# Performance work log

Measured on AMD Instinct MI355X. Metric: run time of the kernel, lower is better.

The kernel has to match this reference:

```python
import jax, jax.numpy as jnp
import numpy as np

B, C, H, W = 8, 512, 64, 64


def _conv1x1(x, w, b):
    # x: (B,C,H,W), w: (O,C,1,1) torch layout, b: (O,)
    y = jnp.einsum('bchw,oc->bohw', x, w[:, :, 0, 0])
    return y + b[None, :, None, None]


def setup_inputs() -> dict:
    key = jax.random.key(0)
    ks = jax.random.split(key, 9)
    s = 1.0 / np.sqrt(C)
    inp = {
        'x': jax.random.normal(ks[0], (B, C, H, W), dtype=jnp.float32),
        'w1': jax.random.uniform(ks[1], (C, C, 1, 1), jnp.float32, -s, s),
        'b1': jax.random.uniform(ks[2], (C,), jnp.float32, -s, s),
        'w2': jax.random.uniform(ks[3], (C, C, 1, 1), jnp.float32, -s, s),
        'b2': jax.random.uniform(ks[4], (C,), jnp.float32, -s, s),
        'w3': jax.random.uniform(ks[5], (C, C, 1, 1), jnp.float32, -s, s),
        'b3': jax.random.uniform(ks[6], (C,), jnp.float32, -s, s),
        'wg': jax.random.uniform(ks[7], (C, 1, 3, 3), jnp.float32, -1.0 / 3.0, 1.0 / 3.0),
        'bg': jax.random.uniform(ks[8], (C,), jnp.float32, -1.0 / 3.0, 1.0 / 3.0),
    }
    return inp


def reference(x, w1, b1, w2, b2, w3, b3, wg, bg):
    q = _conv1x1(x, w1, b1)  # (B,C,H,W)
    k = _conv1x1(x, w2, b2)
    v = _conv1x1(x, w3, b3)
    qf = q.reshape(B, C, H * W)
    kf = k.reshape(B, C, H * W)
    vf = v.reshape(B, C, H * W)
    # channel-wise attention: (B,C,C)
    scores = jnp.einsum('bcn,bdn->bcd', qf, kf)
    attn = jax.nn.softmax(scores, axis=-1)
    denoised = jnp.einsum('bcd,bdn->bcn', attn, vf).reshape(B, C, H, W)
    # depthwise 3x3 conv, padding=1
    local = jax.lax.conv_general_dilated(
        x, wg, window_strides=(1, 1), padding=((1, 1), (1, 1)),
        feature_group_count=C,
        dimension_numbers=('NCHW', 'OIHW', 'NCHW'))
    local = local + bg[None, :, None, None]
    return x + 0.1 * denoised + 0.1 * local
```

## Files before the change

kernel.cpp:

```cpp
#include <hip/hip_runtime.h>

typedef _Float16 f16;
typedef _Float16 half8 __attribute__((ext_vector_type(8)));
typedef _Float16 half4 __attribute__((ext_vector_type(4)));
typedef float    f32x4 __attribute__((ext_vector_type(4)));

#define DEV static __device__ __forceinline__

constexpr int NB = 8, CH = 512, HW = 4096, IH = 64, IW = 64;

typedef const __attribute__((address_space(1))) void gas_void;
typedef __attribute__((address_space(3))) void       las_void;

template <int ROWS>
DEV void stage_gll(f16* lds, const f16* src, long ld) {
  const int lane = threadIdx.x & 63, w = threadIdx.x >> 6;
  const int r8 = lane >> 3, c16 = lane & 7;
#pragma unroll
  for (int i = w; i < (ROWS / 8); i += 4) {
    const f16* g = src + (long)(i * 8 + r8) * ld + c16 * 8;
    __builtin_amdgcn_global_load_lds((gas_void*)g, (las_void*)(lds + i * 512 + lane * 8), 16, 0, 0);
  }
}

template <int BM, int BN, bool SPLIT, int KS, int EPI, bool TRI>
__global__ __launch_bounds__(256, 2) void gemm2(
    const f16* __restrict__ Ah, const f16* __restrict__ Al, long sAb, int lda,
    const f16* __restrict__ Bh, const f16* __restrict__ Bl, long sBb, int ldb,
    void* __restrict__ O1, void* __restrict__ O2, long sOb, int ldo, int K,
    const float* __restrict__ e0, const float* __restrict__ e1,
    const float* __restrict__ e2, const float* __restrict__ e3) {
  constexpr int FM = BM / 32, FN = BN / 32;
  __shared__ f16 sAh[BM * 64], sBh[BN * 64];
  __shared__ f16 sAl[SPLIT ? BM * 64 : 1], sBl[SPLIT ? BN * 64 : 1];

  int bx = blockIdx.x, by = blockIdx.y;
  if constexpr (TRI) {
    int t = blockIdx.x, mi = 0;
    while (t >= 4 - mi) { t -= 4 - mi; ++mi; }
    bx = mi; by = mi + t;
  }
  const int bz = blockIdx.z, b = bz / KS, ks = bz % KS;
  const int m0 = bx * BM, n0 = by * BN;
  const int lane = threadIdx.x & 63, wave = threadIdx.x >> 6;
  const int wr = (wave >> 1) * (BM / 2), wc = (wave & 1) * (BN / 2);
  const int fr = lane & 15, fq = lane >> 4;

  const f16* Ab  = Ah + b * sAb + (long)m0 * lda;
  const f16* Bb  = Bh + b * sBb + (long)n0 * ldb;
  const f16* Ab2 = SPLIT ? Al + b * sAb + (long)m0 * lda : nullptr;
  const f16* Bb2 = SPLIT ? Bl + b * sBb + (long)n0 * ldb : nullptr;

  f32x4 acc[FM][FN] = {};
  const int kbeg = ks * K, kend = kbeg + K;
  for (int k0 = kbeg; k0 < kend; k0 += 64) {
    stage_gll<BM>(sAh, Ab + k0, lda);
    stage_gll<BN>(sBh, Bb + k0, ldb);
    if constexpr (SPLIT) {
      stage_gll<BM>(sAl, Ab2 + k0, lda);
      stage_gll<BN>(sBl, Bb2 + k0, ldb);
    }
    __syncthreads();
#pragma unroll
    for (int kk = 0; kk < 2; ++kk) {
      half8 ah[FM], bh[FN];
#pragma unroll
      for (int mi = 0; mi < FM; ++mi)
        ah[mi] = *(const half8*)&sAh[(wr + mi * 16 + fr) * 64 + kk * 32 + fq * 8];
#pragma unroll
      for (int ni = 0; ni < FN; ++ni)
        bh[ni] = *(const half8*)&sBh[(wc + ni * 16 + fr) * 64 + kk * 32 + fq * 8];
      if constexpr (SPLIT) {
        half8 al[FM], bl[FN];
#pragma unroll
        for (int mi = 0; mi < FM; ++mi)
          al[mi] = *(const half8*)&sAl[(wr + mi * 16 + fr) * 64 + kk * 32 + fq * 8];
#pragma unroll
        for (int ni = 0; ni < FN; ++ni)
          bl[ni] = *(const half8*)&sBl[(wc + ni * 16 + fr) * 64 + kk * 32 + fq * 8];
#pragma unroll
        for (int mi = 0; mi < FM; ++mi)
#pragma unroll
          for (int ni = 0; ni < FN; ++ni) {
            acc[mi][ni] = __builtin_amdgcn_mfma_f32_16x16x32_f16(ah[mi], bh[ni], acc[mi][ni], 0, 0, 0);
            acc[mi][ni] = __builtin_amdgcn_mfma_f32_16x16x32_f16(ah[mi], bl[ni], acc[mi][ni], 0, 0, 0);
            acc[mi][ni] = __builtin_amdgcn_mfma_f32_16x16x32_f16(al[mi], bh[ni], acc[mi][ni], 0, 0, 0);
          }
      } else {
#pragma unroll
        for (int mi = 0; mi < FM; ++mi)
#pragma unroll
          for (int ni = 0; ni < FN; ++ni)
            acc[mi][ni] = __builtin_amdgcn_mfma_f32_16x16x32_f16(ah[mi], bh[ni], acc[mi][ni], 0, 0, 0);
      }
    }
    __syncthreads();
  }

#pragma unroll
  for (int mi = 0; mi < FM; ++mi)
#pragma unroll
    for (int ni = 0; ni < FN; ++ni)
#pragma unroll
      for (int j = 0; j < 4; ++j) {
        const int row = m0 + wr + mi * 16 + fq * 4 + j;
        const int col = n0 + wc + ni * 16 + fr;
        float g = acc[mi][ni][j];
        const long oi = b * sOb + (long)row * ldo + col;
        if constexpr (EPI == 0) {
          f16 h = (f16)g;
          ((f16*)O1)[oi] = h;
          ((f16*)O2)[oi] = (f16)(g - (float)h);
        } else if constexpr (EPI == 1) {
          g += e0[row] * e1[b * CH + col] + e2[b * CH + row] * e3[col];
          ((float*)O1)[oi] = g;
        } else if constexpr (EPI == 2) {
          ((f16*)O1)[oi] = (f16)g;
        } else if constexpr (EPI == 3) {
          ((float*)O1)[oi] += 0.1f * (g + e1[b * CH + row]);
        } else {
          unsafeAtomicAdd(&((float*)O1)[oi], g);
        }
      }
}

template <int OP>
DEV float blockReduce(float v) {
#pragma unroll
  for (int o = 32; o; o >>= 1) {
    float w = __shfl_xor(v, o);
    v = OP ? fmaxf(v, w) : v + w;
  }
  __shared__ float t[4];
  __shared__ float res;
  __syncthreads();
  if ((threadIdx.x & 63) == 0) t[threadIdx.x >> 6] = v;
  __syncthreads();
  if (threadIdx.x == 0)
    res = OP ? fmaxf(fmaxf(t[0], t[1]), fmaxf(t[2], t[3])) : t[0] + t[1] + t[2] + t[3];
  __syncthreads();
  return res;
}

__global__ __launch_bounds__(256) void convert_x(const float* __restrict__ x, f16* __restrict__ xh,
                                                 f16* __restrict__ xl, f16* __restrict__ xT) {
  const int p0 = blockIdx.x * 64, c0 = blockIdx.y * 64, b = blockIdx.z;
  __shared__ f16 tl[64][72];
  const int t = threadIdx.x;
  const int rr0 = t >> 4, c4 = (t & 15) * 4;
  const float* xb = x + (long)b * CH * HW;
#pragma unroll
  for (int i = 0; i < 4; ++i) {
    const int r = rr0 + i * 16;
    f32x4 v = *(const f32x4*)(xb + (long)(c0 + r) * HW + p0 + c4);
    half4 h, l;
#pragma unroll
    for (int j = 0; j < 4; ++j) {
      f16 hi = (f16)v[j];
      h[j] = hi;
      l[j] = (f16)(v[j] - (float)hi);
      tl[c4 + j][r] = hi;
    }
    *(half4*)(xh + ((long)b * CH + c0 + r) * HW + p0 + c4) = h;
    *(half4*)(xl + ((long)b * CH + c0 + r) * HW + p0 + c4) = l;
  }
  __syncthreads();
  const int pr = t >> 2, cc = (t & 3) * 16;
  f16* dst = xT + ((long)b * HW + p0 + pr) * CH + c0 + cc;
  *(half8*)dst       = *(half8*)&tl[pr][cc];
  *(half8*)(dst + 8) = *(half8*)&tl[pr][cc + 8];
}

__global__ __launch_bounds__(256) void cvt_g(const float* __restrict__ G32, f16* __restrict__ Gh,
                                             f16* __restrict__ Gl) {
  const int c0 = blockIdx.x * 64, r0 = blockIdx.y * 64, b = blockIdx.z;
  const bool lower = (r0 >> 7) > (c0 >> 7);
  __shared__ float tl[64][65];
  const int t = threadIdx.x;
  const int rr0 = t >> 4, c4 = (t & 15) * 4;
  const float* Gb = G32 + (long)b * CH * CH;
  if (lower) {
#pragma unroll
    for (int i = 0; i < 4; ++i) {
      const int r = rr0 + i * 16;
      f32x4 v = *(const f32x4*)(Gb + (long)(c0 + r) * CH + r0 + c4);
#pragma unroll
      for (int j = 0; j < 4; ++j) tl[c4 + j][r] = v[j];
    }
    __syncthreads();
  }
#pragma unroll
  for (int i = 0; i < 4; ++i) {
    const int r = rr0 + i * 16;
    f32x4 v;
    if (lower)
      v = *(const f32x4*)&tl[r][c4];
    else
      v = *(const f32x4*)(Gb + (long)(r0 + r) * CH + c0 + c4);
    half4 h, l;
#pragma unroll
    for (int j = 0; j < 4; ++j) {
      f16 hi = (f16)v[j];
      h[j] = hi;
      l[j] = (f16)(v[j] - (float)hi);
    }
    *(half4*)(Gh + ((long)b * CH + r0 + r) * CH + c0 + c4) = h;
    *(half4*)(Gl + ((long)b * CH + r0 + r) * CH + c0 + c4) = l;
  }
}

__global__ __launch_bounds__(256) void prep_w(const float* __restrict__ w1, const float* __restrict__ w2,
                                              const float* __restrict__ w3, f16* w1h, f16* w1l, f16* w2h,
                                              f16* w2l, f16* w3t) {
  const int i = blockIdx.x * 256 + threadIdx.x;
  if (i >= CH * CH) return;
  float a = w1[i];
  f16 h = (f16)a;
  w1h[i] = h;
  w1l[i] = (f16)(a - (float)h);
  float bv = w2[i];
  h = (f16)bv;
  w2h[i] = h;
  w2l[i] = (f16)(bv - (float)h);
  const int r = i >> 9, c = i & 511;
  w3t[c * CH + r] = (f16)w3[i];
}

__global__ __launch_bounds__(256) void rowsum_k(const float* __restrict__ x, float* __restrict__ s) {
  const int b = blockIdx.y, c = blockIdx.x;
  const float* p = x + ((long)(b * CH + c)) * HW;
  float a = 0.f;
  for (int i = threadIdx.x; i < HW; i += 256) a += p[i];
  a = blockReduce<0>(a);
  if (threadIdx.x == 0) s[b * CH + c] = a;
}

__global__ __launch_bounds__(256) void prep_tu(const float* __restrict__ w1, const float* __restrict__ w2,
                                               const float* __restrict__ b2, const float* __restrict__ s,
                                               float* __restrict__ t, float* __restrict__ u) {
  const int b = blockIdx.y, c = blockIdx.x;
  float a1 = 0.f, a2 = 0.f;
  for (int i = threadIdx.x; i < CH; i += 256) {
    float sv = s[b * CH + i];
    a1 += w1[(long)c * CH + i] * sv;
    a2 += w2[(long)c * CH + i] * sv;
  }
  a1 = blockReduce<0>(a1);
  a2 = blockReduce<0>(a2);
  if (threadIdx.x == 0) {
    t[b * CH + c] = a1;
    u[b * CH + c] = a2 + (float)HW * b2[c];
  }
}

__global__ __launch_bounds__(256) void softmax_k(const float* __restrict__ sc, const float* __restrict__ b3,
                                                 f16* __restrict__ attn, float* __restrict__ ab3) {
  const int b = blockIdx.y, c = blockIdx.x;
  const float* row = sc + ((long)(b * CH + c)) * CH;
  const float v0 = row[threadIdx.x], v1 = row[threadIdx.x + 256];
  const float m = blockReduce<1>(fmaxf(v0, v1));
  const float q0 = __expf(v0 - m), q1 = __expf(v1 - m);
  const float sum = blockReduce<0>(q0 + q1);
  const float sb = blockReduce<0>(q0 * b3[threadIdx.x] + q1 * b3[threadIdx.x + 256]);
  const float inv = 1.f / sum;
  attn[((long)(b * CH + c)) * CH + threadIdx.x] = (f16)(q0 * inv);
  attn[((long)(b * CH + c)) * CH + threadIdx.x + 256] = (f16)(q1 * inv);
  if (threadIdx.x == 0) ab3[b * CH + c] = sb * inv;
}

__global__ __launch_bounds__(256) void dwconv_k(const float* __restrict__ x, const float* __restrict__ wg,
                                                const float* __restrict__ bg, float* __restrict__ out) {
  const int b = blockIdx.y, c = blockIdx.x;
  __shared__ float img[IH][IW + 1];
  const float* p = x + ((long)(b * CH + c)) * HW;
  for (int i = threadIdx.x; i < HW; i += 256) img[i >> 6][i & 63] = p[i];
  __syncthreads();
  float w[3][3];
#pragma unroll
  for (int k = 0; k < 9; ++k) w[k / 3][k % 3] = wg[c * 9 + k];
  const float bias = bg[c];
  float* op = out + ((long)(b * CH + c)) * HW;
  for (int i = threadIdx.x; i < HW; i += 256) {
    const int h = i >> 6, ww = i & 63;
    float acc = bias;
#pragma unroll
    for (int dy = -1; dy <= 1; ++dy) {
      const int hh = h + dy;
      if (hh < 0 || hh >= IH) continue;
#pragma unroll
      for (int dx = -1; dx <= 1; ++dx) {
        const int cc2 = ww + dx;
        if (cc2 < 0 || cc2 >= IW) continue;
        acc += w[dy + 1][dx + 1] * img[hh][cc2];
      }
    }
    op[i] = img[h][ww] + 0.1f * acc;
  }
}

extern "C" void kernel_launch(void* const* d_in, const int* in_sizes, int n_in, void* d_out, int out_size,
                              void* d_ws, size_t ws_size, hipStream_t stream) {
  const float* x  = (const float*)d_in[0];
  const float* w1 = (const float*)d_in[1];
  const float* b1 = (const float*)d_in[2];
  const float* w2 = (const float*)d_in[3];
  const float* b2 = (const float*)d_in[4];
  const float* w3 = (const float*)d_in[5];
  const float* b3 = (const float*)d_in[6];
  const float* wg = (const float*)d_in[7];
  const float* bg = (const float*)d_in[8];
  float* out = (float*)d_out;

  char* ws = (char*)d_ws;
  size_t off = 0;
  auto alloc = [&](size_t bytes) -> void* {
    void* p = ws + off;
    off += (bytes + 255) & ~(size_t)255;
    return p;
  };
  const long CC = (long)CH * CH;
  const long CHW = (long)CH * HW;
  f16* xh  = (f16*)alloc(NB * CHW * 2);
  f16* xl  = (f16*)alloc(NB * CHW * 2);
  f16* xT  = (f16*)alloc(NB * CHW * 2);
  float* G32 = (float*)alloc(NB * CC * 4);
  f16* G16h = (f16*)alloc(NB * CC * 2);
  f16* G16l = (f16*)alloc(NB * CC * 2);
  f16* P16h = (f16*)alloc(NB * CC * 2);
  f16* P16l = (f16*)alloc(NB * CC * 2);
  f16* w1h = (f16*)alloc(CC * 2);
  f16* w1l = (f16*)alloc(CC * 2);
  f16* w2h = (f16*)alloc(CC * 2);
  f16* w2l = (f16*)alloc(CC * 2);
  f16* w3t = (f16*)alloc(CC * 2);
  float* sv = (float*)alloc(NB * CH * 4);
  float* tv = (float*)alloc(NB * CH * 4);
  float* uv = (float*)alloc(NB * CH * 4);
  float* ab3 = (float*)alloc(NB * CH * 4);
  float* scores = G32;
  f16* attn16 = G16h;
  f16* M16    = G16l;

  const dim3 blk(256);

  prep_w<<<dim3((CH * CH + 255) / 256), blk, 0, stream>>>(w1, w2, w3, w1h, w1l, w2h, w2l, w3t);
  convert_x<<<dim3(HW / 64, CH / 64, NB), blk, 0, stream>>>(x, xh, xl, xT);
  rowsum_k<<<dim3(CH, NB), blk, 0, stream>>>(x, sv);
  prep_tu<<<dim3(CH, NB), blk, 0, stream>>>(w1, w2, b2, sv, tv, uv);
  hipMemsetAsync(G32, 0, NB * CC * 4, stream);

  gemm2<128, 128, true, 8, 5, true><<<dim3(10, 1, NB * 8), blk, 0, stream>>>(
      xh, xl, CHW, HW, xh, xl, CHW, HW, G32, nullptr, CC, CH, HW / 8,
      nullptr, nullptr, nullptr, nullptr);
  cvt_g<<<dim3(8, 8, NB), blk, 0, stream>>>(G32, G16h, G16l);
  gemm2<128, 64, true, 1, 0, false><<<dim3(4, 8, NB), blk, 0, stream>>>(
      w1h, w1l, 0, CH, G16h, G16l, CC, CH, P16h, P16l, CC, CH, CH,
      nullptr, nullptr, nullptr, nullptr);
  gemm2<128, 64, true, 1, 1, false><<<dim3(4, 8, NB), blk, 0, stream>>>(
      P16h, P16l, CC, CH, w2h, w2l, 0, CH, scores, nullptr, CC, CH, CH, b1, uv, tv, b2);
  softmax_k<<<dim3(CH, NB), blk, 0, stream>>>(scores, b3, attn16, ab3);
  gemm2<128, 64, false, 1, 2, false><<<dim3(4, 8, NB), blk, 0, stream>>>(
      attn16, nullptr, CC, CH, w3t, nullptr, 0, CH, M16, nullptr, CC, CH, CH,
      nullptr, nullptr, nullptr, nullptr);
  dwconv_k<<<dim3(CH, NB), blk, 0, stream>>>(x, wg, bg, out);
  gemm2<128, 128, false, 1, 3, false><<<dim3(4, HW / 128, NB), blk, 0, stream>>>(
      M16, nullptr, CC, CH, xT, nullptr, CHW, CH, out, nullptr, CHW, HW, CH,
      nullptr, ab3, nullptr, nullptr);
}
```

Before: 381.7 us.

## Fuse rowsum into convert_x, reuse A tile on diagonal, fold dwconv into combine

The per-channel row sums move into convert_x as shuffle reductions plus atomics, which removes a separate full pass over x. Diagonal blocks of the symmetric Gram GEMM reuse the A tile in LDS for B instead of loading the same data twice. The final GEMM now writes the denoised result to an fp16 buffer (reusing xl), and a new combine kernel adds it to the depthwise conv, bias and residual. This drops the read-modify-write of out inside the GEMM epilogue, at the cost of an extra fp16 intermediate round trip and some precision loss from rounding the denoised term to fp16.

```diff
diff --git a/kernel.cpp b/kernel.cpp
--- a/kernel.cpp
+++ b/kernel.cpp
@@ -40,6 +40,7 @@
     while (t >= 4 - mi) { t -= 4 - mi; ++mi; }
     bx = mi; by = mi + t;
   }
+  const bool diag = TRI && (bx == by);
   const int bz = blockIdx.z, b = bz / KS, ks = bz % KS;
   const int m0 = bx * BM, n0 = by * BN;
   const int lane = threadIdx.x & 63, wave = threadIdx.x >> 6;
@@ -51,14 +52,17 @@
   const f16* Ab2 = SPLIT ? Al + b * sAb + (long)m0 * lda : nullptr;
   const f16* Bb2 = SPLIT ? Bl + b * sBb + (long)n0 * ldb : nullptr;
 
+  const f16* pBh = diag ? sAh : sBh;
+  const f16* pBl = diag ? sAl : sBl;
+
   f32x4 acc[FM][FN] = {};
   const int kbeg = ks * K, kend = kbeg + K;
   for (int k0 = kbeg; k0 < kend; k0 += 64) {
     stage_gll<BM>(sAh, Ab + k0, lda);
-    stage_gll<BN>(sBh, Bb + k0, ldb);
+    if (!diag) stage_gll<BN>(sBh, Bb + k0, ldb);
     if constexpr (SPLIT) {
       stage_gll<BM>(sAl, Ab2 + k0, lda);
-      stage_gll<BN>(sBl, Bb2 + k0, ldb);
+      if (!diag) stage_gll<BN>(sBl, Bb2 + k0, ldb);
     }
     __syncthreads();
 #pragma unroll
@@ -69,7 +73,7 @@
         ah[mi] = *(const half8*)&sAh[(wr + mi * 16 + fr) * 64 + kk * 32 + fq * 8];
 #pragma unroll
       for (int ni = 0; ni < FN; ++ni)
-        bh[ni] = *(const half8*)&sBh[(wc + ni * 16 + fr) * 64 + kk * 32 + fq * 8];
+        bh[ni] = *(const half8*)&pBh[(wc + ni * 16 + fr) * 64 + kk * 32 + fq * 8];
       if constexpr (SPLIT) {
         half8 al[FM], bl[FN];
 #pragma unroll
@@ -77,7 +81,7 @@
           al[mi] = *(const half8*)&sAl[(wr + mi * 16 + fr) * 64 + kk * 32 + fq * 8];
 #pragma unroll
         for (int ni = 0; ni < FN; ++ni)
-          bl[ni] = *(const half8*)&sBl[(wc + ni * 16 + fr) * 64 + kk * 32 + fq * 8];
+          bl[ni] = *(const half8*)&pBl[(wc + ni * 16 + fr) * 64 + kk * 32 + fq * 8];
 #pragma unroll
         for (int mi = 0; mi < FM; ++mi)
 #pragma unroll
@@ -116,8 +120,6 @@
           ((float*)O1)[oi] = g;
         } else if constexpr (EPI == 2) {
           ((f16*)O1)[oi] = (f16)g;
-        } else if constexpr (EPI == 3) {
-          ((float*)O1)[oi] += 0.1f * (g + e1[b * CH + row]);
         } else {
           unsafeAtomicAdd(&((float*)O1)[oi], g);
         }
@@ -143,7 +145,8 @@
 }
 
 __global__ __launch_bounds__(256) void convert_x(const float* __restrict__ x, f16* __restrict__ xh,
-                                                 f16* __restrict__ xl, f16* __restrict__ xT) {
+                                                 f16* __restrict__ xl, f16* __restrict__ xT,
+                                                 float* __restrict__ sv) {
   const int p0 = blockIdx.x * 64, c0 = blockIdx.y * 64, b = blockIdx.z;
   __shared__ f16 tl[64][72];
   const int t = threadIdx.x;
@@ -163,6 +166,12 @@
     }
     *(half4*)(xh + ((long)b * CH + c0 + r) * HW + p0 + c4) = h;
     *(half4*)(xl + ((long)b * CH + c0 + r) * HW + p0 + c4) = l;
+    float s4 = v[0] + v[1] + v[2] + v[3];
+    s4 += __shfl_xor(s4, 1);
+    s4 += __shfl_xor(s4, 2);
+    s4 += __shfl_xor(s4, 4);
+    s4 += __shfl_xor(s4, 8);
+    if ((t & 15) == 0) unsafeAtomicAdd(&sv[(long)b * CH + c0 + r], s4);
   }
   __syncthreads();
   const int pr = t >> 2, cc = (t & 3) * 16;
@@ -226,15 +235,6 @@
   w3t[c * CH + r] = (f16)w3[i];
 }
 
-__global__ __launch_bounds__(256) void rowsum_k(const float* __restrict__ x, float* __restrict__ s) {
-  const int b = blockIdx.y, c = blockIdx.x;
-  const float* p = x + ((long)(b * CH + c)) * HW;
-  float a = 0.f;
-  for (int i = threadIdx.x; i < HW; i += 256) a += p[i];
-  a = blockReduce<0>(a);
-  if (threadIdx.x == 0) s[b * CH + c] = a;
-}
-
 __global__ __launch_bounds__(256) void prep_tu(const float* __restrict__ w1, const float* __restrict__ w2,
                                                const float* __restrict__ b2, const float* __restrict__ s,
                                                float* __restrict__ t, float* __restrict__ u) {
@@ -268,8 +268,9 @@
   if (threadIdx.x == 0) ab3[b * CH + c] = sb * inv;
 }
 
-__global__ __launch_bounds__(256) void dwconv_k(const float* __restrict__ x, const float* __restrict__ wg,
-                                                const float* __restrict__ bg, float* __restrict__ out) {
+__global__ __launch_bounds__(256) void combine_k(const float* __restrict__ x, const f16* __restrict__ den,
+                                                 const float* __restrict__ wg, const float* __restrict__ bg,
+                                                 const float* __restrict__ ab3, float* __restrict__ out) {
   const int b = blockIdx.y, c = blockIdx.x;
   __shared__ float img[IH][IW + 1];
   const float* p = x + ((long)(b * CH + c)) * HW;
@@ -278,11 +279,12 @@
   float w[3][3];
 #pragma unroll
   for (int k = 0; k < 9; ++k) w[k / 3][k % 3] = wg[c * 9 + k];
-  const float bias = bg[c];
+  const float base = bg[c] + ab3[b * CH + c];
+  const f16* dp = den + ((long)(b * CH + c)) * HW;
   float* op = out + ((long)(b * CH + c)) * HW;
   for (int i = threadIdx.x; i < HW; i += 256) {
     const int h = i >> 6, ww = i & 63;
-    float acc = bias;
+    float acc = base + (float)dp[i];
 #pragma unroll
     for (int dy = -1; dy <= 1; ++dy) {
       const int hh = h + dy;
@@ -340,12 +342,13 @@
   float* scores = G32;
   f16* attn16 = G16h;
   f16* M16    = G16l;
+  f16* den16  = xl;
 
   const dim3 blk(256);
 
   prep_w<<<dim3((CH * CH + 255) / 256), blk, 0, stream>>>(w1, w2, w3, w1h, w1l, w2h, w2l, w3t);
-  convert_x<<<dim3(HW / 64, CH / 64, NB), blk, 0, stream>>>(x, xh, xl, xT);
-  rowsum_k<<<dim3(CH, NB), blk, 0, stream>>>(x, sv);
+  hipMemsetAsync(sv, 0, NB * CH * 4, stream);
+  convert_x<<<dim3(HW / 64, CH / 64, NB), blk, 0, stream>>>(x, xh, xl, xT, sv);
   prep_tu<<<dim3(CH, NB), blk, 0, stream>>>(w1, w2, b2, sv, tv, uv);
   hipMemsetAsync(G32, 0, NB * CC * 4, stream);
 
@@ -362,8 +365,8 @@
   gemm2<128, 64, false, 1, 2, false><<<dim3(4, 8, NB), blk, 0, stream>>>(
       attn16, nullptr, CC, CH, w3t, nullptr, 0, CH, M16, nullptr, CC, CH, CH,
       nullptr, nullptr, nullptr, nullptr);
-  dwconv_k<<<dim3(CH, NB), blk, 0, stream>>>(x, wg, bg, out);
-  gemm2<128, 128, false, 1, 3, false><<<dim3(4, HW / 128, NB), blk, 0, stream>>>(
-      M16, nullptr, CC, CH, xT, nullptr, CHW, CH, out, nullptr, CHW, HW, CH,
-      nullptr, ab3, nullptr, nullptr);
-}
+  gemm2<128, 128, false, 1, 2, false><<<dim3(4, HW / 128, NB), blk, 0, stream>>>(
+      M16, nullptr, CC, CH, xT, nullptr, CHW, CH, den16, nullptr, CHW, HW, CH,
+      nullptr, nullptr, nullptr, nullptr);
+  combine_k<<<dim3(CH, NB), blk, 0, stream>>>(x, den16, wg, bg, ab3, out);
+}
```

Result: faster. 344.5 us (-9.8%).

## Compute Gram matrix with single fp16 GEMM using hi/mid split and partial buffers

Applied to the files above, without the earlier changes.

Replaces the split-precision triangular Gram GEMM (hi/lo for both operands, atomics into a zeroed buffer) with one non-split GEMM of xh against xm, where xm = 2x - xh. This makes xh·xm + xm·xh ≈ 2·x·x^T once symmetrised. Split-K partials go to separate buffers and cvt_g sums them with their transposes. The row-sum is fused into the conversion kernel, and the final GEMM writes denoised fp16 into a combine kernel that also applies the depthwise conv and bias. The aim is to cut GEMM work, the memset and the atomics. The trade-offs are a full (non-triangular) grid, extra partial-buffer traffic and fp16 rounding of xm and of the denoised output.

```diff
diff --git a/kernel.cpp b/kernel.cpp
--- a/kernel.cpp
+++ b/kernel.cpp
@@ -23,7 +23,7 @@
   }
 }
 
-template <int BM, int BN, bool SPLIT, int KS, int EPI, bool TRI>
+template <int BM, int BN, bool SPLIT, int KS, int EPI>
 __global__ __launch_bounds__(256, 2) void gemm2(
     const f16* __restrict__ Ah, const f16* __restrict__ Al, long sAb, int lda,
     const f16* __restrict__ Bh, const f16* __restrict__ Bl, long sBb, int ldb,
@@ -34,12 +34,7 @@
   __shared__ f16 sAh[BM * 64], sBh[BN * 64];
   __shared__ f16 sAl[SPLIT ? BM * 64 : 1], sBl[SPLIT ? BN * 64 : 1];
 
-  int bx = blockIdx.x, by = blockIdx.y;
-  if constexpr (TRI) {
-    int t = blockIdx.x, mi = 0;
-    while (t >= 4 - mi) { t -= 4 - mi; ++mi; }
-    bx = mi; by = mi + t;
-  }
+  const int bx = blockIdx.x, by = blockIdx.y;
   const int bz = blockIdx.z, b = bz / KS, ks = bz % KS;
   const int m0 = bx * BM, n0 = by * BN;
   const int lane = threadIdx.x & 63, wave = threadIdx.x >> 6;
@@ -116,10 +111,8 @@
           ((float*)O1)[oi] = g;
         } else if constexpr (EPI == 2) {
           ((f16*)O1)[oi] = (f16)g;
-        } else if constexpr (EPI == 3) {
-          ((float*)O1)[oi] += 0.1f * (g + e1[b * CH + row]);
         } else {
-          unsafeAtomicAdd(&((float*)O1)[oi], g);
+          ((float*)O1)[(((long)ks * NB + b) * CH + row) * CH + col] = g;
         }
       }
 }
@@ -142,70 +135,90 @@
   return res;
 }
 
-__global__ __launch_bounds__(256) void convert_x(const float* __restrict__ x, f16* __restrict__ xh,
-                                                 f16* __restrict__ xl, f16* __restrict__ xT) {
+__global__ __launch_bounds__(256) void convert1(const float* __restrict__ x, f16* __restrict__ xh,
+                                                f16* __restrict__ xm, float* __restrict__ sv) {
+  const int c = blockIdx.x, b = blockIdx.y;
+  const long base = ((long)(b * CH + c)) * HW;
+  const float* p = x + base;
+  f16* ph = xh + base;
+  f16* pm = xm + base;
+  float s = 0.f;
+#pragma unroll
+  for (int i0 = 0; i0 < 4; ++i0) {
+    const int i = (threadIdx.x + i0 * 256) * 4;
+    f32x4 v = *(const f32x4*)(p + i);
+    half4 h, m;
+#pragma unroll
+    for (int j = 0; j < 4; ++j) {
+      f16 hi = (f16)v[j];
+      h[j] = hi;
+      m[j] = (f16)(2.f * v[j] - (float)hi);
+      s += v[j];
+    }
+    *(half4*)(ph + i) = h;
+    *(half4*)(pm + i) = m;
+  }
+  s = blockReduce<0>(s);
+  if (threadIdx.x == 0) sv[b * CH + c] = s;
+}
+
+__global__ __launch_bounds__(256) void convert2(const f16* __restrict__ xh, f16* __restrict__ xT) {
   const int p0 = blockIdx.x * 64, c0 = blockIdx.y * 64, b = blockIdx.z;
   __shared__ f16 tl[64][72];
   const int t = threadIdx.x;
-  const int rr0 = t >> 4, c4 = (t & 15) * 4;
-  const float* xb = x + (long)b * CH * HW;
-#pragma unroll
-  for (int i = 0; i < 4; ++i) {
-    const int r = rr0 + i * 16;
-    f32x4 v = *(const f32x4*)(xb + (long)(c0 + r) * HW + p0 + c4);
-    half4 h, l;
-#pragma unroll
-    for (int j = 0; j < 4; ++j) {
-      f16 hi = (f16)v[j];
-      h[j] = hi;
-      l[j] = (f16)(v[j] - (float)hi);
-      tl[c4 + j][r] = hi;
-    }
-    *(half4*)(xh + ((long)b * CH + c0 + r) * HW + p0 + c4) = h;
-    *(half4*)(xl + ((long)b * CH + c0 + r) * HW + p0 + c4) = l;
-  }
-  __syncthreads();
-  const int pr = t >> 2, cc = (t & 3) * 16;
-  f16* dst = xT + ((long)b * HW + p0 + pr) * CH + c0 + cc;
-  *(half8*)dst       = *(half8*)&tl[pr][cc];
-  *(half8*)(dst + 8) = *(half8*)&tl[pr][cc + 8];
-}
-
-__global__ __launch_bounds__(256) void cvt_g(const float* __restrict__ G32, f16* __restrict__ Gh,
+  const int cr = t >> 2, pc = (t & 3) * 16;
+  const f16* src = xh + ((long)(b * CH) + c0 + cr) * HW + p0 + pc;
+  half8 a0 = *(const half8*)src, a1 = *(const half8*)(src + 8);
+#pragma unroll
+  for (int j = 0; j < 8; ++j) {
+    tl[pc + j][cr] = a0[j];
+    tl[pc + 8 + j][cr] = a1[j];
+  }
+  __syncthreads();
+  f16* dst = xT + ((long)b * HW + p0 + cr) * CH + c0 + pc;
+  *(half8*)dst       = *(half8*)&tl[cr][pc];
+  *(half8*)(dst + 8) = *(half8*)&tl[cr][pc + 8];
+}
+
+template <int KS>
+__global__ __launch_bounds__(256) void cvt_g(const float* __restrict__ E, f16* __restrict__ Gh,
                                              f16* __restrict__ Gl) {
   const int c0 = blockIdx.x * 64, r0 = blockIdx.y * 64, b = blockIdx.z;
-  const bool lower = (r0 >> 7) > (c0 >> 7);
   __shared__ float tl[64][65];
   const int t = threadIdx.x;
   const int rr0 = t >> 4, c4 = (t & 15) * 4;
-  const float* Gb = G32 + (long)b * CH * CH;
-  if (lower) {
+  f32x4 acc[4] = {};
+  for (int ks = 0; ks < KS; ++ks) {
+    const float* Eb = E + ((long)ks * NB + b) * (long)CH * CH;
+#pragma unroll
+    for (int i = 0; i < 4; ++i)
+      acc[i] += *(const f32x4*)(Eb + (long)(r0 + rr0 + i * 16) * CH + c0 + c4);
+    __syncthreads();
 #pragma unroll
     for (int i = 0; i < 4; ++i) {
-      const int r = rr0 + i * 16;
-      f32x4 v = *(const f32x4*)(Gb + (long)(c0 + r) * CH + r0 + c4);
-#pragma unroll
-      for (int j = 0; j < 4; ++j) tl[c4 + j][r] = v[j];
+      f32x4 w = *(const f32x4*)(Eb + (long)(c0 + rr0 + i * 16) * CH + r0 + c4);
+#pragma unroll
+      for (int j = 0; j < 4; ++j) tl[rr0 + i * 16][c4 + j] = w[j];
     }
     __syncthreads();
+#pragma unroll
+    for (int i = 0; i < 4; ++i)
+#pragma unroll
+      for (int j = 0; j < 4; ++j) acc[i][j] += tl[c4 + j][rr0 + i * 16];
   }
 #pragma unroll
   for (int i = 0; i < 4; ++i) {
-    const int r = rr0 + i * 16;
-    f32x4 v;
-    if (lower)
-      v = *(const f32x4*)&tl[r][c4];
-    else
-      v = *(const f32x4*)(Gb + (long)(r0 + r) * CH + c0 + c4);
     half4 h, l;
 #pragma unroll
     for (int j = 0; j < 4; ++j) {
-      f16 hi = (f16)v[j];
+      const float g = 0.5f * acc[i][j];
+      f16 hi = (f16)g;
       h[j] = hi;
-      l[j] = (f16)(v[j] - (float)hi);
-    }
-    *(half4*)(Gh + ((long)b * CH + r0 + r) * CH + c0 + c4) = h;
-    *(half4*)(Gl + ((long)b * CH + r0 + r) * CH + c0 + c4) = l;
+      l[j] = (f16)(g - (float)hi);
+    }
+    const long oi = ((long)b * CH + r0 + rr0 + i * 16) * CH + c0 + c4;
+    *(half4*)(Gh + oi) = h;
+    *(half4*)(Gl + oi) = l;
   }
 }
 
@@ -226,15 +239,6 @@
   w3t[c * CH + r] = (f16)w3[i];
 }
 
-__global__ __launch_bounds__(256) void rowsum_k(const float* __restrict__ x, float* __restrict__ s) {
-  const int b = blockIdx.y, c = blockIdx.x;
-  const float* p = x + ((long)(b * CH + c)) * HW;
-  float a = 0.f;
-  for (int i = threadIdx.x; i < HW; i += 256) a += p[i];
-  a = blockReduce<0>(a);
-  if (threadIdx.x == 0) s[b * CH + c] = a;
-}
-
 __global__ __launch_bounds__(256) void prep_tu(const float* __restrict__ w1, const float* __restrict__ w2,
                                                const float* __restrict__ b2, const float* __restrict__ s,
                                                float* __restrict__ t, float* __restrict__ u) {
@@ -268,33 +272,48 @@
   if (threadIdx.x == 0) ab3[b * CH + c] = sb * inv;
 }
 
-__global__ __launch_bounds__(256) void dwconv_k(const float* __restrict__ x, const float* __restrict__ wg,
-                                                const float* __restrict__ bg, float* __restrict__ out) {
+__global__ __launch_bounds__(256) void combine_k(const float* __restrict__ x, const f16* __restrict__ den,
+                                                 const float* __restrict__ wg, const float* __restrict__ bg,
+                                                 const float* __restrict__ ab3, float* __restrict__ out) {
   const int b = blockIdx.y, c = blockIdx.x;
-  __shared__ float img[IH][IW + 1];
-  const float* p = x + ((long)(b * CH + c)) * HW;
-  for (int i = threadIdx.x; i < HW; i += 256) img[i >> 6][i & 63] = p[i];
+  __shared__ float img[IH][IW + 4];
+  const long base = ((long)(b * CH + c)) * HW;
+  const float* p = x + base;
+  const int t = threadIdx.x;
+  const int h0 = t >> 2, w0 = (t & 3) * 16;
+#pragma unroll
+  for (int k = 0; k < 4; ++k)
+    *(f32x4*)&img[h0][w0 + 4 * k] = *(const f32x4*)(p + h0 * 64 + w0 + 4 * k);
   __syncthreads();
   float w[3][3];
 #pragma unroll
   for (int k = 0; k < 9; ++k) w[k / 3][k % 3] = wg[c * 9 + k];
-  const float bias = bg[c];
-  float* op = out + ((long)(b * CH + c)) * HW;
-  for (int i = threadIdx.x; i < HW; i += 256) {
-    const int h = i >> 6, ww = i & 63;
-    float acc = bias;
-#pragma unroll
-    for (int dy = -1; dy <= 1; ++dy) {
-      const int hh = h + dy;
-      if (hh < 0 || hh >= IH) continue;
-#pragma unroll
-      for (int dx = -1; dx <= 1; ++dx) {
-        const int cc2 = ww + dx;
-        if (cc2 < 0 || cc2 >= IW) continue;
-        acc += w[dy + 1][dx + 1] * img[hh][cc2];
+  const float bb = bg[c] + ab3[b * CH + c];
+  const f16* dp = den + base;
+  float* op = out + base;
+#pragma unroll
+  for (int k = 0; k < 4; ++k) {
+    const int ww = w0 + 4 * k;
+    half4 d4 = *(const half4*)(dp + h0 * 64 + ww);
+    f32x4 o;
+#pragma unroll
+    for (int j = 0; j < 4; ++j) {
+      const int wj = ww + j;
+      float acc = bb + (float)d4[j];
+#pragma unroll
+      for (int dy = -1; dy <= 1; ++dy) {
+        const int hh = h0 + dy;
+        if (hh < 0 || hh >= IH) continue;
+#pragma unroll
+        for (int dx = -1; dx <= 1; ++dx) {
+          const int cc2 = wj + dx;
+          if (cc2 < 0 || cc2 >= IW) continue;
+          acc += w[dy + 1][dx + 1] * img[hh][cc2];
+        }
       }
-    }
-    op[i] = img[h][ww] + 0.1f * acc;
+      o[j] = img[h0][wj] + 0.1f * acc;
+    }
+    *(f32x4*)(op + h0 * 64 + ww) = o;
   }
 }
 
@@ -320,10 +339,10 @@
   };
   const long CC = (long)CH * CH;
   const long CHW = (long)CH * HW;
-  f16* xh  = (f16*)alloc(NB * CHW * 2);
-  f16* xl  = (f16*)alloc(NB * CHW * 2);
-  f16* xT  = (f16*)alloc(NB * CHW * 2);
-  float* G32 = (float*)alloc(NB * CC * 4);
+  constexpr int GKS = 4;
+  f16* xh    = (f16*)alloc(NB * CHW * 2);
+  f16* xm    = (f16*)alloc(NB * CHW * 2);
+  float* Epart = (float*)alloc((long)GKS * NB * CC * 4);
   f16* G16h = (f16*)alloc(NB * CC * 2);
   f16* G16l = (f16*)alloc(NB * CC * 2);
   f16* P16h = (f16*)alloc(NB * CC * 2);
@@ -337,33 +356,34 @@
   float* tv = (float*)alloc(NB * CH * 4);
   float* uv = (float*)alloc(NB * CH * 4);
   float* ab3 = (float*)alloc(NB * CH * 4);
-  float* scores = G32;
-  f16* attn16 = G16h;
-  f16* M16    = G16l;
+  f16* xT     = (f16*)Epart;
+  float* scores = (float*)xh;
+  f16* attn16 = (f16*)((char*)xh + (NB * CC * 4));
+  f16* M16    = (f16*)((char*)xh + (NB * CC * 4) + (NB * CC * 2));
+  f16* den16  = xm;
 
   const dim3 blk(256);
 
   prep_w<<<dim3((CH * CH + 255) / 256), blk, 0, stream>>>(w1, w2, w3, w1h, w1l, w2h, w2l, w3t);
-  convert_x<<<dim3(HW / 64, CH / 64, NB), blk, 0, stream>>>(x, xh, xl, xT);
-  rowsum_k<<<dim3(CH, NB), blk, 0, stream>>>(x, sv);
+  convert1<<<dim3(CH, NB), blk, 0, stream>>>(x, xh, xm, sv);
   prep_tu<<<dim3(CH, NB), blk, 0, stream>>>(w1, w2, b2, sv, tv, uv);
-  hipMemsetAsync(G32, 0, NB * CC * 4, stream);
-
-  gemm2<128, 128, true, 8, 5, true><<<dim3(10, 1, NB * 8), blk, 0, stream>>>(
-      xh, xl, CHW, HW, xh, xl, CHW, HW, G32, nullptr, CC, CH, HW / 8,
+
+  gemm2<128, 128, false, GKS, 6><<<dim3(4, 4, NB * GKS), blk, 0, stream>>>(
+      xh, nullptr, CHW, HW, xm, nullptr, CHW, HW, Epart, nullptr, CC, CH, HW / GKS,
       nullptr, nullptr, nullptr, nullptr);
-  cvt_g<<<dim3(8, 8, NB), blk, 0, stream>>>(G32, G16h, G16l);
-  gemm2<128, 64, true, 1, 0, false><<<dim3(4, 8, NB), blk, 0, stream>>>(
+  cvt_g<GKS><<<dim3(8, 8, NB), blk, 0, stream>>>(Epart, G16h, G16l);
+  convert2<<<dim3(HW / 64, CH / 64, NB), blk, 0, stream>>>(xh, xT);
+  gemm2<128, 64, true, 1, 0><<<dim3(4, 8, NB), blk, 0, stream>>>(
       w1h, w1l, 0, CH, G16h, G16l, CC, CH, P16h, P16l, CC, CH, CH,
       nullptr, nullptr, nullptr, nullptr);
-  gemm2<128, 64, true, 1, 1, false><<<dim3(4, 8, NB), blk, 0, stream>>>(
+  gemm2<128, 64, true, 1, 1><<<dim3(4, 8, NB), blk, 0, stream>>>(
       P16h, P16l, CC, CH, w2h, w2l, 0, CH, scores, nullptr, CC, CH, CH, b1, uv, tv, b2);
   softmax_k<<<dim3(CH, NB), blk, 0, stream>>>(scores, b3, attn16, ab3);
-  gemm2<128, 64, false, 1, 2, false><<<dim3(4, 8, NB), blk, 0, stream>>>(
+  gemm2<128, 64, false, 1, 2><<<dim3(4, 8, NB), blk, 0, stream>>>(
       attn16, nullptr, CC, CH, w3t, nullptr, 0, CH, M16, nullptr, CC, CH, CH,
       nullptr, nullptr, nullptr, nullptr);
-  dwconv_k<<<dim3(CH, NB), blk, 0, stream>>>(x, wg, bg, out);
-  gemm2<128, 128, false, 1, 3, false><<<dim3(4, HW / 128, NB), blk, 0, stream>>>(
-      M16, nullptr, CC, CH, xT, nullptr, CHW, CH, out, nullptr, CHW, HW, CH,
-      nullptr, ab3, nullptr, nullptr);
-}
+  gemm2<128, 128, false, 1, 2><<<dim3(4, HW / 128, NB), blk, 0, stream>>>(
+      M16, nullptr, CC, CH, xT, nullptr, CHW, CH, den16, nullptr, CHW, HW, CH,
+      nullptr, nullptr, nullptr, nullptr);
+  combine_k<<<dim3(CH, NB), blk, 0, stream>>>(x, den16, wg, bg, ab3, out);
+}
```

Measured after the change: 337.0 us. 1.13x faster.
